# Optimization experiments

Measured on AMD Instinct MI355X. Metric: run time of the kernel, lower is better.

Reference implementation:

```python
import jax, jax.numpy as jnp
import numpy as np

B = 8192        # batch
OBS = 256       # obs_dim
ACT = 32        # action_dim -> output is 2*ACT (mu, log_std)
HID = 512       # hidden_dim
P = 8           # number of base policies (experts)
LOG_STD_MIN, LOG_STD_MAX = -5.0, 2.0


def setup_inputs() -> dict:
    key = jax.random.key(0)
    ks = jax.random.split(key, 14)
    s = 0.05
    return {
        "obs": jax.random.normal(ks[0], (B, OBS), dtype=jnp.float32),
        # gate network: obs -> HID -> HID -> P (softmax)
        "gw0": jax.random.normal(ks[1], (HID, OBS), dtype=jnp.float32) * s,
        "gb0": jnp.zeros((HID,), dtype=jnp.float32),
        "gw1": jax.random.normal(ks[2], (HID, HID), dtype=jnp.float32) * s,
        "gb1": jnp.zeros((HID,), dtype=jnp.float32),
        "gw2": jax.random.normal(ks[3], (P, HID), dtype=jnp.float32) * s,
        "gb2": jnp.zeros((P,), dtype=jnp.float32),
        # stacked expert (base-policy) trunk params, hidden_depth=2
        "ew0": jax.random.normal(ks[4], (P, HID, OBS), dtype=jnp.float32) * s,
        "eb0": jax.random.normal(ks[5], (P, HID), dtype=jnp.float32) * s,
        "ew1": jax.random.normal(ks[6], (P, HID, HID), dtype=jnp.float32) * s,
        "eb1": jax.random.normal(ks[7], (P, HID), dtype=jnp.float32) * s,
        "ew2": jax.random.normal(ks[8], (P, 2 * ACT, HID), dtype=jnp.float32) * s,
        "eb2": jax.random.normal(ks[9], (P, 2 * ACT), dtype=jnp.float32) * s,
    }


def _blend_linear(blend, W, b, x):
    # Math identical to: W_new = reshape(blend @ flatten(W,1)); bmm(W_new, x) + blend @ b
    # Contracted in the efficient order (per-expert GEMM then blend): [B,P,out] intermediate.
    y = jnp.einsum('bp,poi,bi->bo', blend, W, x, optimize=True)
    return y + blend @ b


def reference(obs, gw0, gb0, gw1, gb1, gw2, gb2, ew0, eb0, ew1, eb1, ew2, eb2):
    # gate network with softmax output
    h = jax.nn.relu(obs @ gw0.T + gb0)
    h = jax.nn.relu(h @ gw1.T + gb1)
    blend = jax.nn.softmax(h @ gw2.T + gb2, axis=-1)  # [B, P]

    # blended per-sample MLP (hidden_depth = 2)
    x = jax.nn.relu(_blend_linear(blend, ew0, eb0, obs))
    x = jax.nn.relu(_blend_linear(blend, ew1, eb1, x))
    x = _blend_linear(blend, ew2, eb2, x)  # [B, 2*ACT]

    mu, log_std = jnp.split(x, 2, axis=-1)
    log_std = jnp.tanh(log_std)
    log_std = LOG_STD_MIN + 0.5 * (LOG_STD_MAX - LOG_STD_MIN) * (log_std + 1.0)
    std = jnp.exp(log_std)
    # dist = SquashedNormal(mu, std); return its defining tensors
    return jnp.concatenate([mu, std], axis=-1)
```

## Files before the change

kernel.cpp:

```cpp
#include <hip/hip_runtime.h>
#include <hip/hip_bf16.h>
#include <cstdint>
#include <cstddef>

#define B_DIM   8192
#define OBS_DIM 256
#define ACT_DIM 32
#define HID_DIM 512
#define NEXPERT 8

typedef __attribute__((ext_vector_type(4))) float        f32x4;
typedef __attribute__((ext_vector_type(8))) short        s16x8;
typedef __attribute__((ext_vector_type(4))) unsigned int u32x4;

__device__ __forceinline__ unsigned cvt_pk_bf16(float lo, float hi) {
    unsigned r;
    asm("v_cvt_pk_bf16_f32 %0, %1, %2" : "=v"(r) : "v"(lo), "v"(hi));
    return r;
}
__device__ __forceinline__ float bf16_lo_f32(unsigned u) { return __uint_as_float(u << 16); }
__device__ __forceinline__ float bf16_hi_f32(unsigned u) { return __uint_as_float(u & 0xffff0000u); }

struct CvtArgs {
    const float*    s[7];
    unsigned short* d[7];
    int             nb[7];
};

__global__ __launch_bounds__(256) void cvt_multi(CvtArgs a) {
    int bid = blockIdx.x;
    int seg = 0, base = 0;
    while (seg < 6 && bid >= base + a.nb[seg]) { base += a.nb[seg]; ++seg; }
    int local = (bid - base) * 256 + threadIdx.x;
    const f32x4* s = (const f32x4*)a.s[seg];
    f32x4 v0 = s[local * 2 + 0];
    f32x4 v1 = s[local * 2 + 1];
    u32x4 o;
    o[0] = cvt_pk_bf16(v0[0], v0[1]);
    o[1] = cvt_pk_bf16(v0[2], v0[3]);
    o[2] = cvt_pk_bf16(v1[0], v1[1]);
    o[3] = cvt_pk_bf16(v1[2], v1[3]);
    ((u32x4*)a.d[seg])[local] = o;
}

__global__ __launch_bounds__(256) void gate_softmax(const unsigned short* __restrict__ h1,
                                                    const unsigned short* __restrict__ gw2,
                                                    const float* __restrict__ gb2,
                                                    float* __restrict__ blend) {
    const int lane = threadIdx.x & 63;
    const int wid  = threadIdx.x >> 6;
    const int row  = blockIdx.x * 4 + wid;

    u32x4 xv = *(const u32x4*)(h1 + (size_t)row * HID_DIM + lane * 8);
    float x[8];
#pragma unroll
    for (int j = 0; j < 4; ++j) {
        unsigned u   = xv[j];
        x[2 * j]     = bf16_lo_f32(u);
        x[2 * j + 1] = bf16_hi_f32(u);
    }
    float s[NEXPERT];
#pragma unroll
    for (int pp = 0; pp < NEXPERT; ++pp) {
        u32x4 wv = *(const u32x4*)(gw2 + (size_t)pp * HID_DIM + lane * 8);
        float d  = 0.f;
#pragma unroll
        for (int j = 0; j < 4; ++j) {
            unsigned u = wv[j];
            d += x[2 * j] * bf16_lo_f32(u);
            d += x[2 * j + 1] * bf16_hi_f32(u);
        }
        s[pp] = d;
    }
#pragma unroll
    for (int off = 1; off < 64; off <<= 1) {
#pragma unroll
        for (int pp = 0; pp < NEXPERT; ++pp) s[pp] += __shfl_xor(s[pp], off);
    }
    if (lane == 0) {
        float l[NEXPERT], m = -1e30f;
#pragma unroll
        for (int pp = 0; pp < NEXPERT; ++pp) { l[pp] = s[pp] + gb2[pp]; m = fmaxf(m, l[pp]); }
        float sum = 0.f;
#pragma unroll
        for (int pp = 0; pp < NEXPERT; ++pp) { l[pp] = __expf(l[pp] - m); sum += l[pp]; }
        float inv = 1.f / sum;
#pragma unroll
        for (int pp = 0; pp < NEXPERT; ++pp) blend[(size_t)row * NEXPERT + pp] = l[pp] * inv;
    }
}

template <int KIN, int NOUT>
__global__ __launch_bounds__(256, 2) void gemm_gate(const unsigned short* __restrict__ A,
                                                    const unsigned short* __restrict__ W,
                                                    const float* __restrict__ bias,
                                                    unsigned short* __restrict__ outb) {
    constexpr int BM = 128, BN = 64, BK = 64;

    __shared__ unsigned short sA[BM * BK];
    __shared__ unsigned short sB[BN * BK];

    const int t    = threadIdx.x;
    const int lane = t & 63;
    const int wid  = t >> 6;
    const int wm   = wid >> 1, wn = wid & 1;
    const int m0   = blockIdx.x * BM;
    const int n0   = blockIdx.y * BN;

    f32x4 acc[4][2];
#pragma unroll
    for (int i = 0; i < 4; ++i)
#pragma unroll
        for (int j = 0; j < 2; ++j) acc[i][j] = {0.f, 0.f, 0.f, 0.f};

#pragma unroll 1
    for (int kt = 0; kt < KIN / BK; ++kt) {
        const int ks = kt * BK;
        __syncthreads();
        const unsigned short* Wp = W + (size_t)n0 * KIN + ks;
#pragma unroll
        for (int c = 0; c < 2; ++c) {
            const int ch  = c * 256 + t;
            const int row = ch >> 3;
            const int gs  = (ch & 7) ^ (row & 7);
            __builtin_amdgcn_global_load_lds(
                (const __attribute__((address_space(1))) unsigned int*)(Wp + (size_t)row * KIN + gs * 8),
                (__attribute__((address_space(3))) unsigned int*)(sB + ch * 8), 16, 0, 0);
        }
        const unsigned short* Ap = A + (size_t)m0 * KIN + ks;
#pragma unroll
        for (int c = 0; c < 4; ++c) {
            const int ch  = c * 256 + t;
            const int row = ch >> 3;
            const int gs  = (ch & 7) ^ (row & 7);
            __builtin_amdgcn_global_load_lds(
                (const __attribute__((address_space(1))) unsigned int*)(Ap + (size_t)row * KIN + gs * 8),
                (__attribute__((address_space(3))) unsigned int*)(sA + ch * 8), 16, 0, 0);
        }
        __syncthreads();

#pragma unroll
        for (int kk = 0; kk < BK; kk += 32) {
            const int kb = kk + ((lane >> 4) << 3);
            s16x8 af[4], bfr[2];
#pragma unroll
            for (int mf = 0; mf < 4; ++mf) {
                const int row = wm * 64 + mf * 16 + (lane & 15);
                const int idx = (row * BK + kb) ^ ((row & 7) << 3);
                af[mf] = *(const s16x8*)(sA + idx);
            }
#pragma unroll
            for (int nf = 0; nf < 2; ++nf) {
                const int row = wn * 32 + nf * 16 + (lane & 15);
                const int idx = (row * BK + kb) ^ ((row & 7) << 3);
                bfr[nf] = *(const s16x8*)(sB + idx);
            }
#pragma unroll
            for (int mf = 0; mf < 4; ++mf)
#pragma unroll
                for (int nf = 0; nf < 2; ++nf)
                    acc[mf][nf] = __builtin_amdgcn_mfma_f32_16x16x32_bf16(af[mf], bfr[nf],
                                                                          acc[mf][nf], 0, 0, 0);
        }
    }

    const int cn = lane & 15;
    const int rb = (lane >> 4) << 2;
#pragma unroll
    for (int nf = 0; nf < 2; ++nf) {
        const int gn   = n0 + wn * 32 + nf * 16 + cn;
        const float bv = bias[gn];
#pragma unroll
        for (int mf = 0; mf < 4; ++mf) {
#pragma unroll
            for (int r = 0; r < 4; ++r) {
                const int gm = m0 + wm * 64 + mf * 16 + rb + r;
                float v = fmaxf(acc[mf][nf][r] + bv, 0.f);
                outb[(size_t)gm * NOUT + gn] = (unsigned short)(cvt_pk_bf16(v, v) & 0xffffu);
            }
        }
    }
}

template <int KIN, int NOUT, int BN, int KTILES>
__global__ __launch_bounds__(256, 2) void gemm_moe_sk(const unsigned short* __restrict__ A,
                                                      const unsigned short* __restrict__ W,
                                                      const float* __restrict__ blend,
                                                      float* __restrict__ part) {
    constexpr int BM   = 128, BK = 64;
    constexpr int NF   = BN / 32;
    constexpr int EXPT = KIN / BK;
    constexpr int NPE  = KTILES / EXPT;
    static_assert(KTILES % EXPT == 0, "split must align to expert boundary");

    __shared__ unsigned short sA[BM * BK];
    __shared__ unsigned short sB[BN * BK];

    const int t    = threadIdx.x;
    const int lane = t & 63;
    const int wid  = t >> 6;
    const int wm   = wid >> 1, wn = wid & 1;
    const int m0   = blockIdx.x * BM;
    const int n0   = blockIdx.y * BN;
    const int sp   = blockIdx.z;

    const int cn = lane & 15;
    const int rb = (lane >> 4) << 2;

    f32x4 mast[4][NF];
#pragma unroll
    for (int i = 0; i < 4; ++i)
#pragma unroll
        for (int j = 0; j < NF; ++j) mast[i][j] = {0.f, 0.f, 0.f, 0.f};

#pragma unroll 1
    for (int pe = 0; pe < NPE; ++pe) {
        const int p = sp * NPE + pe;
        f32x4 eacc[4][NF];
#pragma unroll
        for (int i = 0; i < 4; ++i)
#pragma unroll
            for (int j = 0; j < NF; ++j) eacc[i][j] = {0.f, 0.f, 0.f, 0.f};

        const unsigned short* Ap0 = A + (size_t)m0 * KIN;
        const unsigned short* Wp0 = W + ((size_t)p * NOUT + n0) * KIN;

#pragma unroll 1
        for (int kt = 0; kt < EXPT; ++kt) {
            const int ks = kt * BK;
            __syncthreads();
#pragma unroll
            for (int c = 0; c < NF; ++c) {
                const int ch  = c * 256 + t;
                const int row = ch >> 3;
                const int gs  = (ch & 7) ^ (row & 7);
                __builtin_amdgcn_global_load_lds(
                    (const __attribute__((address_space(1))) unsigned int*)(Wp0 + (size_t)row * KIN + ks + gs * 8),
                    (__attribute__((address_space(3))) unsigned int*)(sB + ch * 8), 16, 0, 0);
            }
#pragma unroll
            for (int c = 0; c < 4; ++c) {
                const int ch  = c * 256 + t;
                const int row = ch >> 3;
                const int gs  = (ch & 7) ^ (row & 7);
                __builtin_amdgcn_global_load_lds(
                    (const __attribute__((address_space(1))) unsigned int*)(Ap0 + (size_t)row * KIN + ks + gs * 8),
                    (__attribute__((address_space(3))) unsigned int*)(sA + ch * 8), 16, 0, 0);
            }
            __syncthreads();

#pragma unroll
            for (int kk = 0; kk < BK; kk += 32) {
                const int kb = kk + ((lane >> 4) << 3);
                s16x8 af[4], bfr[NF];
#pragma unroll
                for (int mf = 0; mf < 4; ++mf) {
                    const int row = wm * 64 + mf * 16 + (lane & 15);
                    const int idx = (row * BK + kb) ^ ((row & 7) << 3);
                    af[mf] = *(const s16x8*)(sA + idx);
                }
#pragma unroll
                for (int nf = 0; nf < NF; ++nf) {
                    const int row = wn * (BN / 2) + nf * 16 + (lane & 15);
                    const int idx = (row * BK + kb) ^ ((row & 7) << 3);
                    bfr[nf] = *(const s16x8*)(sB + idx);
                }
#pragma unroll
                for (int mf = 0; mf < 4; ++mf)
#pragma unroll
                    for (int nf = 0; nf < NF; ++nf)
                        eacc[mf][nf] = __builtin_amdgcn_mfma_f32_16x16x32_bf16(af[mf], bfr[nf],
                                                                               eacc[mf][nf], 0, 0, 0);
            }
        }

#pragma unroll
        for (int mf = 0; mf < 4; ++mf) {
#pragma unroll
            for (int r = 0; r < 4; ++r) {
                const int gm = m0 + wm * 64 + mf * 16 + rb + r;
                const float bl = blend[(size_t)gm * NEXPERT + p];
#pragma unroll
                for (int nf = 0; nf < NF; ++nf)
                    mast[mf][nf][r] += bl * eacc[mf][nf][r];
            }
        }
    }

    float* dst = part + (size_t)sp * B_DIM * NOUT;
#pragma unroll
    for (int mf = 0; mf < 4; ++mf) {
#pragma unroll
        for (int r = 0; r < 4; ++r) {
            const int gm = m0 + wm * 64 + mf * 16 + rb + r;
#pragma unroll
            for (int nf = 0; nf < NF; ++nf) {
                const int gn = n0 + wn * (BN / 2) + nf * 16 + cn;
                dst[(size_t)gm * NOUT + gn] = mast[mf][nf][r];
            }
        }
    }
}

__global__ __launch_bounds__(256) void reduce2_relu(const float* __restrict__ part,
                                                    const float* __restrict__ blend,
                                                    const float* __restrict__ eb,
                                                    unsigned short* __restrict__ out) {
    const int tid = blockIdx.x * 256 + threadIdx.x;
    const int row = tid >> 6;
    const int c0  = (tid & 63) << 3;

    const f32x4* p0 = (const f32x4*)(part + (size_t)row * HID_DIM + c0);
    const f32x4* p1 = (const f32x4*)(part + ((size_t)B_DIM + row) * HID_DIM + c0);
    f32x4 v0 = p0[0], v1 = p0[1], w0 = p1[0], w1 = p1[1];

    const f32x4* bl = (const f32x4*)(blend + (size_t)row * NEXPERT);
    const f32x4 b0 = bl[0], b1 = bl[1];
    const float blv[8] = {b0[0], b0[1], b0[2], b0[3], b1[0], b1[1], b1[2], b1[3]};

    float res[8];
#pragma unroll
    for (int j = 0; j < 4; ++j) { res[j] = v0[j] + w0[j]; res[4 + j] = v1[j] + w1[j]; }
#pragma unroll
    for (int pp = 0; pp < NEXPERT; ++pp) {
        const f32x4* e = (const f32x4*)(eb + (size_t)pp * HID_DIM + c0);
        const f32x4 e0 = e[0], e1 = e[1];
#pragma unroll
        for (int j = 0; j < 4; ++j) {
            res[j]     += blv[pp] * e0[j];
            res[4 + j] += blv[pp] * e1[j];
        }
    }
    u32x4 o;
#pragma unroll
    for (int j = 0; j < 4; ++j)
        o[j] = cvt_pk_bf16(fmaxf(res[2 * j], 0.f), fmaxf(res[2 * j + 1], 0.f));
    *(u32x4*)(out + (size_t)row * HID_DIM + c0) = o;
}

__global__ __launch_bounds__(256) void reduce8_head(const float* __restrict__ part,
                                                    const float* __restrict__ blend,
                                                    const float* __restrict__ eb2,
                                                    float* __restrict__ out) {
    const int tid = blockIdx.x * 256 + threadIdx.x;
    const int row = tid >> 3;
    const int c0  = (tid & 7) << 3;

    float res[8] = {0.f, 0.f, 0.f, 0.f, 0.f, 0.f, 0.f, 0.f};
#pragma unroll
    for (int sp = 0; sp < 8; ++sp) {
        const f32x4* ps = (const f32x4*)(part + ((size_t)sp * B_DIM + row) * 64 + c0);
        const f32x4 a = ps[0], b = ps[1];
#pragma unroll
        for (int j = 0; j < 4; ++j) { res[j] += a[j]; res[4 + j] += b[j]; }
    }
    const f32x4* bl = (const f32x4*)(blend + (size_t)row * NEXPERT);
    const f32x4 b0 = bl[0], b1 = bl[1];
    const float blv[8] = {b0[0], b0[1], b0[2], b0[3], b1[0], b1[1], b1[2], b1[3]};
#pragma unroll
    for (int pp = 0; pp < NEXPERT; ++pp) {
        const f32x4* e = (const f32x4*)(eb2 + (size_t)pp * 64 + c0);
        const f32x4 e0 = e[0], e1 = e[1];
#pragma unroll
        for (int j = 0; j < 4; ++j) {
            res[j]     += blv[pp] * e0[j];
            res[4 + j] += blv[pp] * e1[j];
        }
    }
    f32x4 o0, o1;
#pragma unroll
    for (int j = 0; j < 8; ++j) {
        const int col = c0 + j;
        float v = res[j];
        if (col >= ACT_DIM) {
            const float vc = fminf(fmaxf(v, -15.f), 15.f);
            const float e2 = __expf(2.f * vc);
            const float th = (e2 - 1.f) / (e2 + 1.f);
            v = __expf(-1.5f + 3.5f * th);
        }
        if (j < 4) o0[j] = v; else o1[j - 4] = v;
    }
    f32x4* dst = (f32x4*)(out + (size_t)row * 64 + c0);
    dst[0] = o0;
    dst[1] = o1;
}

extern "C" void kernel_launch(void* const* d_in, const int* in_sizes, int n_in,
                              void* d_out, int out_size, void* d_ws, size_t ws_size,
                              hipStream_t stream) {
    const float* obs = (const float*)d_in[0];
    const float* gw0 = (const float*)d_in[1];
    const float* gb0 = (const float*)d_in[2];
    const float* gw1 = (const float*)d_in[3];
    const float* gb1 = (const float*)d_in[4];
    const float* gw2 = (const float*)d_in[5];
    const float* gb2 = (const float*)d_in[6];
    const float* ew0 = (const float*)d_in[7];
    const float* eb0 = (const float*)d_in[8];
    const float* ew1 = (const float*)d_in[9];
    const float* eb1 = (const float*)d_in[10];
    const float* ew2 = (const float*)d_in[11];
    const float* eb2 = (const float*)d_in[12];

    char* w = (char*)d_ws;
    auto alloc = [&](size_t bytes) {
        char* r = w;
        w += (bytes + 255) & ~(size_t)255;
        return r;
    };
    unsigned short* obs_bf = (unsigned short*)alloc((size_t)B_DIM * OBS_DIM * 2);
    unsigned short* gw0_bf = (unsigned short*)alloc((size_t)HID_DIM * OBS_DIM * 2);
    unsigned short* gw1_bf = (unsigned short*)alloc((size_t)HID_DIM * HID_DIM * 2);
    unsigned short* gw2_bf = (unsigned short*)alloc((size_t)NEXPERT * HID_DIM * 2);
    unsigned short* ew0_bf = (unsigned short*)alloc((size_t)NEXPERT * HID_DIM * OBS_DIM * 2);
    unsigned short* ew1_bf = (unsigned short*)alloc((size_t)NEXPERT * HID_DIM * HID_DIM * 2);
    unsigned short* ew2_bf = (unsigned short*)alloc((size_t)NEXPERT * 2 * ACT_DIM * HID_DIM * 2);
    unsigned short* h0     = (unsigned short*)alloc((size_t)B_DIM * HID_DIM * 2);
    unsigned short* h1     = (unsigned short*)alloc((size_t)B_DIM * HID_DIM * 2);
    float*          blend  = (float*)alloc((size_t)B_DIM * NEXPERT * 4);
    float*          part   = (float*)alloc((size_t)2 * B_DIM * HID_DIM * 4);

    CvtArgs ca;
    ca.s[0] = obs; ca.d[0] = obs_bf; ca.nb[0] = (B_DIM * OBS_DIM / 8) / 256;
    ca.s[1] = gw0; ca.d[1] = gw0_bf; ca.nb[1] = (HID_DIM * OBS_DIM / 8) / 256;
    ca.s[2] = gw1; ca.d[2] = gw1_bf; ca.nb[2] = (HID_DIM * HID_DIM / 8) / 256;
    ca.s[3] = gw2; ca.d[3] = gw2_bf; ca.nb[3] = (NEXPERT * HID_DIM / 8) / 256;
    ca.s[4] = ew0; ca.d[4] = ew0_bf; ca.nb[4] = (NEXPERT * HID_DIM * OBS_DIM / 8) / 256;
    ca.s[5] = ew1; ca.d[5] = ew1_bf; ca.nb[5] = (NEXPERT * HID_DIM * HID_DIM / 8) / 256;
    ca.s[6] = ew2; ca.d[6] = ew2_bf; ca.nb[6] = (NEXPERT * 64 * HID_DIM / 8) / 256;
    int total_blocks = 0;
    for (int i = 0; i < 7; ++i) total_blocks += ca.nb[i];
    cvt_multi<<<total_blocks, 256, 0, stream>>>(ca);

    gemm_gate<OBS_DIM, HID_DIM><<<dim3(B_DIM / 128, HID_DIM / 64), 256, 0, stream>>>(
        obs_bf, gw0_bf, gb0, h0);
    gemm_gate<HID_DIM, HID_DIM><<<dim3(B_DIM / 128, HID_DIM / 64), 256, 0, stream>>>(
        h0, gw1_bf, gb1, h1);
    gate_softmax<<<B_DIM / 4, 256, 0, stream>>>(h1, gw2_bf, gb2, blend);

    gemm_moe_sk<OBS_DIM, HID_DIM, 128, 16><<<dim3(B_DIM / 128, HID_DIM / 128, 2), 256, 0, stream>>>(
        obs_bf, ew0_bf, blend, part);
    reduce2_relu<<<B_DIM * 64 / 256, 256, 0, stream>>>(part, blend, eb0, h0);

    gemm_moe_sk<HID_DIM, HID_DIM, 128, 32><<<dim3(B_DIM / 128, HID_DIM / 128, 2), 256, 0, stream>>>(
        h0, ew1_bf, blend, part);
    reduce2_relu<<<B_DIM * 64 / 256, 256, 0, stream>>>(part, blend, eb1, h1);

    gemm_moe_sk<HID_DIM, 64, 64, 8><<<dim3(B_DIM / 128, 1, 8), 256, 0, stream>>>(
        h1, ew2_bf, blend, part);
    reduce8_head<<<B_DIM * 8 / 256, 256, 0, stream>>>(part, blend, eb2, (float*)d_out);
}
```

Before: 214.8 us.

## Fuse all stages into one persistent kernel with software grid barriers

Replaces the ten separate launches (convert, two gate GEMMs, softmax, three MoE GEMMs, three reductions) with a single persistent kernel of 512 blocks. The stages are separated by atomic-counter grid barriers, and each block strides over its virtual blocks. The aim is to remove per-launch overhead and the gaps between dependent kernels. The risks are barrier spin cost and a dependence on all 512 blocks being co-resident at two blocks per CU. The barrier also has a timeout break that could silently race if co-residency fails.

```diff
diff --git a/kernel.cpp b/kernel.cpp
--- a/kernel.cpp
+++ b/kernel.cpp
@@ -8,6 +8,7 @@
 #define ACT_DIM 32
 #define HID_DIM 512
 #define NEXPERT 8
+#define GRID    512
 
 typedef __attribute__((ext_vector_type(4))) float        f32x4;
 typedef __attribute__((ext_vector_type(8))) short        s16x8;
@@ -21,91 +22,68 @@
 __device__ __forceinline__ float bf16_lo_f32(unsigned u) { return __uint_as_float(u << 16); }
 __device__ __forceinline__ float bf16_hi_f32(unsigned u) { return __uint_as_float(u & 0xffff0000u); }
 
-struct CvtArgs {
-    const float*    s[7];
-    unsigned short* d[7];
-    int             nb[7];
+struct MegaArgs {
+    const float*    cs[7];
+    unsigned short* cd[7];
+    int             cnb[7];
+    int             ctot;
+    const unsigned short *obs_bf, *gw0_bf, *gw1_bf, *gw2_bf, *ew0_bf, *ew1_bf, *ew2_bf;
+    const float *gb0, *gb1, *gb2, *eb0, *eb1, *eb2;
+    unsigned short *h0, *h1;
+    float *blend, *part, *out;
+    unsigned *bar;
 };
 
-__global__ __launch_bounds__(256) void cvt_multi(CvtArgs a) {
-    int bid = blockIdx.x;
-    int seg = 0, base = 0;
-    while (seg < 6 && bid >= base + a.nb[seg]) { base += a.nb[seg]; ++seg; }
-    int local = (bid - base) * 256 + threadIdx.x;
-    const f32x4* s = (const f32x4*)a.s[seg];
-    f32x4 v0 = s[local * 2 + 0];
-    f32x4 v1 = s[local * 2 + 1];
-    u32x4 o;
-    o[0] = cvt_pk_bf16(v0[0], v0[1]);
-    o[1] = cvt_pk_bf16(v0[2], v0[3]);
-    o[2] = cvt_pk_bf16(v1[0], v1[1]);
-    o[3] = cvt_pk_bf16(v1[2], v1[3]);
-    ((u32x4*)a.d[seg])[local] = o;
-}
-
-__global__ __launch_bounds__(256) void gate_softmax(const unsigned short* __restrict__ h1,
-                                                    const unsigned short* __restrict__ gw2,
-                                                    const float* __restrict__ gb2,
-                                                    float* __restrict__ blend) {
-    const int lane = threadIdx.x & 63;
-    const int wid  = threadIdx.x >> 6;
-    const int row  = blockIdx.x * 4 + wid;
-
-    u32x4 xv = *(const u32x4*)(h1 + (size_t)row * HID_DIM + lane * 8);
-    float x[8];
-#pragma unroll
-    for (int j = 0; j < 4; ++j) {
-        unsigned u   = xv[j];
-        x[2 * j]     = bf16_lo_f32(u);
-        x[2 * j + 1] = bf16_hi_f32(u);
-    }
-    float s[NEXPERT];
-#pragma unroll
-    for (int pp = 0; pp < NEXPERT; ++pp) {
-        u32x4 wv = *(const u32x4*)(gw2 + (size_t)pp * HID_DIM + lane * 8);
-        float d  = 0.f;
-#pragma unroll
-        for (int j = 0; j < 4; ++j) {
-            unsigned u = wv[j];
-            d += x[2 * j] * bf16_lo_f32(u);
-            d += x[2 * j + 1] * bf16_hi_f32(u);
-        }
-        s[pp] = d;
-    }
-#pragma unroll
-    for (int off = 1; off < 64; off <<= 1) {
-#pragma unroll
-        for (int pp = 0; pp < NEXPERT; ++pp) s[pp] += __shfl_xor(s[pp], off);
-    }
-    if (lane == 0) {
-        float l[NEXPERT], m = -1e30f;
-#pragma unroll
-        for (int pp = 0; pp < NEXPERT; ++pp) { l[pp] = s[pp] + gb2[pp]; m = fmaxf(m, l[pp]); }
-        float sum = 0.f;
-#pragma unroll
-        for (int pp = 0; pp < NEXPERT; ++pp) { l[pp] = __expf(l[pp] - m); sum += l[pp]; }
-        float inv = 1.f / sum;
-#pragma unroll
-        for (int pp = 0; pp < NEXPERT; ++pp) blend[(size_t)row * NEXPERT + pp] = l[pp] * inv;
+__device__ __forceinline__ void grid_barrier(unsigned* ctr) {
+    __syncthreads();
+    if (threadIdx.x == 0) {
+        __threadfence();
+        atomicAdd(ctr, 1u);
+        const long long t0 = clock64();
+        while (__hip_atomic_load(ctr, __ATOMIC_RELAXED, __HIP_MEMORY_SCOPE_AGENT)
+               < (unsigned)GRID) {
+            __builtin_amdgcn_s_sleep(2);
+            if (clock64() - t0 > (1LL << 26)) break;
+        }
+        __threadfence();
+    }
+    __syncthreads();
+}
+
+__device__ void cvt_stage(int b, const MegaArgs& a) {
+    const int t = threadIdx.x;
+    for (int vb = b; vb < a.ctot; vb += GRID) {
+        int seg = 0, base = 0;
+        while (seg < 6 && vb >= base + a.cnb[seg]) { base += a.cnb[seg]; ++seg; }
+        const int local = (vb - base) * 256 + t;
+        const f32x4* s = (const f32x4*)a.cs[seg];
+        f32x4 v0 = s[local * 2 + 0];
+        f32x4 v1 = s[local * 2 + 1];
+        u32x4 o;
+        o[0] = cvt_pk_bf16(v0[0], v0[1]);
+        o[1] = cvt_pk_bf16(v0[2], v0[3]);
+        o[2] = cvt_pk_bf16(v1[0], v1[1]);
+        o[3] = cvt_pk_bf16(v1[2], v1[3]);
+        ((u32x4*)a.cd[seg])[local] = o;
     }
 }
 
 template <int KIN, int NOUT>
-__global__ __launch_bounds__(256, 2) void gemm_gate(const unsigned short* __restrict__ A,
-                                                    const unsigned short* __restrict__ W,
-                                                    const float* __restrict__ bias,
-                                                    unsigned short* __restrict__ outb) {
+__device__ void gate_stage(int b, const unsigned short* __restrict__ A,
+                           const unsigned short* __restrict__ W,
+                           const float* __restrict__ bias,
+                           unsigned short* __restrict__ outb,
+                           unsigned char* SMEM) {
     constexpr int BM = 128, BN = 64, BK = 64;
-
-    __shared__ unsigned short sA[BM * BK];
-    __shared__ unsigned short sB[BN * BK];
+    unsigned short* sA = (unsigned short*)SMEM;
+    unsigned short* sB = (unsigned short*)(SMEM + BM * BK * 2);
 
     const int t    = threadIdx.x;
     const int lane = t & 63;
     const int wid  = t >> 6;
     const int wm   = wid >> 1, wn = wid & 1;
-    const int m0   = blockIdx.x * BM;
-    const int n0   = blockIdx.y * BN;
+    const int m0   = (b & 63) * BM;
+    const int n0   = (b >> 6) * BN;
 
     f32x4 acc[4][2];
 #pragma unroll
@@ -182,27 +160,77 @@
     }
 }
 
-template <int KIN, int NOUT, int BN, int KTILES>
-__global__ __launch_bounds__(256, 2) void gemm_moe_sk(const unsigned short* __restrict__ A,
-                                                      const unsigned short* __restrict__ W,
-                                                      const float* __restrict__ blend,
-                                                      float* __restrict__ part) {
-    constexpr int BM   = 128, BK = 64;
-    constexpr int NF   = BN / 32;
-    constexpr int EXPT = KIN / BK;
-    constexpr int NPE  = KTILES / EXPT;
-    static_assert(KTILES % EXPT == 0, "split must align to expert boundary");
-
-    __shared__ unsigned short sA[BM * BK];
-    __shared__ unsigned short sB[BN * BK];
+__device__ void softmax_stage(int b, const unsigned short* __restrict__ h1,
+                              const unsigned short* __restrict__ gw2,
+                              const float* __restrict__ gb2,
+                              float* __restrict__ blend) {
+    const int lane = threadIdx.x & 63;
+    const int wid  = threadIdx.x >> 6;
+    for (int vb = b; vb < B_DIM / 4; vb += GRID) {
+        const int row = vb * 4 + wid;
+        u32x4 xv = *(const u32x4*)(h1 + (size_t)row * HID_DIM + lane * 8);
+        float x[8];
+#pragma unroll
+        for (int j = 0; j < 4; ++j) {
+            unsigned u   = xv[j];
+            x[2 * j]     = bf16_lo_f32(u);
+            x[2 * j + 1] = bf16_hi_f32(u);
+        }
+        float s[NEXPERT];
+#pragma unroll
+        for (int pp = 0; pp < NEXPERT; ++pp) {
+            u32x4 wv = *(const u32x4*)(gw2 + (size_t)pp * HID_DIM + lane * 8);
+            float d  = 0.f;
+#pragma unroll
+            for (int j = 0; j < 4; ++j) {
+                unsigned u = wv[j];
+                d += x[2 * j] * bf16_lo_f32(u);
+                d += x[2 * j + 1] * bf16_hi_f32(u);
+            }
+            s[pp] = d;
+        }
+#pragma unroll
+        for (int off = 1; off < 64; off <<= 1) {
+#pragma unroll
+            for (int pp = 0; pp < NEXPERT; ++pp) s[pp] += __shfl_xor(s[pp], off);
+        }
+        if (lane == 0) {
+            float l[NEXPERT], m = -1e30f;
+#pragma unroll
+            for (int pp = 0; pp < NEXPERT; ++pp) { l[pp] = s[pp] + gb2[pp]; m = fmaxf(m, l[pp]); }
+            float sum = 0.f;
+#pragma unroll
+            for (int pp = 0; pp < NEXPERT; ++pp) { l[pp] = __expf(l[pp] - m); sum += l[pp]; }
+            float inv = 1.f / sum;
+#pragma unroll
+            for (int pp = 0; pp < NEXPERT; ++pp) blend[(size_t)row * NEXPERT + pp] = l[pp] * inv;
+        }
+    }
+}
+
+template <int KIN, int NOUT, int BN, int TPB>
+__device__ void moe_stage(int b, const unsigned short* __restrict__ A,
+                          const unsigned short* __restrict__ W,
+                          const float* __restrict__ blend,
+                          float* __restrict__ part,
+                          unsigned char* SMEM) {
+    constexpr int BM  = 128, BK = 64;
+    constexpr int NF  = BN / 32;
+    constexpr int TPE = KIN / BK;
+    constexpr int NPE = (TPB >= TPE) ? TPB / TPE : 1;
+    constexpr int ET  = (TPB >= TPE) ? TPE : TPB;
+    static_assert((TPB % TPE == 0) || (TPE % TPB == 0), "split/expert alignment");
+
+    unsigned short* sA = (unsigned short*)SMEM;
+    unsigned short* sB = (unsigned short*)(SMEM + BM * BK * 2);
 
     const int t    = threadIdx.x;
     const int lane = t & 63;
     const int wid  = t >> 6;
     const int wm   = wid >> 1, wn = wid & 1;
-    const int m0   = blockIdx.x * BM;
-    const int n0   = blockIdx.y * BN;
-    const int sp   = blockIdx.z;
+    const int m0 = (b & 63) * BM;
+    const int n0 = (NOUT == 64) ? 0 : ((b >> 6) & 3) * BN;
+    const int sp = (NOUT == 64) ? (b >> 6) : (b >> 8);
 
     const int cn = lane & 15;
     const int rb = (lane >> 4) << 2;
@@ -215,18 +243,21 @@
 
 #pragma unroll 1
     for (int pe = 0; pe < NPE; ++pe) {
-        const int p = sp * NPE + pe;
+        const int tbase = sp * TPB + pe * ET;
+        const int p     = tbase / TPE;
+        const int ksb   = (tbase % TPE) * BK;
+
         f32x4 eacc[4][NF];
 #pragma unroll
         for (int i = 0; i < 4; ++i)
 #pragma unroll
             for (int j = 0; j < NF; ++j) eacc[i][j] = {0.f, 0.f, 0.f, 0.f};
 
-        const unsigned short* Ap0 = A + (size_t)m0 * KIN;
-        const unsigned short* Wp0 = W + ((size_t)p * NOUT + n0) * KIN;
+        const unsigned short* Ap0 = A + (size_t)m0 * KIN + ksb;
+        const unsigned short* Wp0 = W + ((size_t)p * NOUT + n0) * KIN + ksb;
 
 #pragma unroll 1
-        for (int kt = 0; kt < EXPT; ++kt) {
+        for (int kt = 0; kt < ET; ++kt) {
             const int ks = kt * BK;
             __syncthreads();
 #pragma unroll
@@ -302,87 +333,116 @@
     }
 }
 
-__global__ __launch_bounds__(256) void reduce2_relu(const float* __restrict__ part,
-                                                    const float* __restrict__ blend,
-                                                    const float* __restrict__ eb,
-                                                    unsigned short* __restrict__ out) {
-    const int tid = blockIdx.x * 256 + threadIdx.x;
-    const int row = tid >> 6;
-    const int c0  = (tid & 63) << 3;
-
-    const f32x4* p0 = (const f32x4*)(part + (size_t)row * HID_DIM + c0);
-    const f32x4* p1 = (const f32x4*)(part + ((size_t)B_DIM + row) * HID_DIM + c0);
-    f32x4 v0 = p0[0], v1 = p0[1], w0 = p1[0], w1 = p1[1];
-
-    const f32x4* bl = (const f32x4*)(blend + (size_t)row * NEXPERT);
-    const f32x4 b0 = bl[0], b1 = bl[1];
-    const float blv[8] = {b0[0], b0[1], b0[2], b0[3], b1[0], b1[1], b1[2], b1[3]};
-
-    float res[8];
-#pragma unroll
-    for (int j = 0; j < 4; ++j) { res[j] = v0[j] + w0[j]; res[4 + j] = v1[j] + w1[j]; }
-#pragma unroll
-    for (int pp = 0; pp < NEXPERT; ++pp) {
-        const f32x4* e = (const f32x4*)(eb + (size_t)pp * HID_DIM + c0);
-        const f32x4 e0 = e[0], e1 = e[1];
-#pragma unroll
-        for (int j = 0; j < 4; ++j) {
-            res[j]     += blv[pp] * e0[j];
-            res[4 + j] += blv[pp] * e1[j];
-        }
-    }
-    u32x4 o;
-#pragma unroll
-    for (int j = 0; j < 4; ++j)
-        o[j] = cvt_pk_bf16(fmaxf(res[2 * j], 0.f), fmaxf(res[2 * j + 1], 0.f));
-    *(u32x4*)(out + (size_t)row * HID_DIM + c0) = o;
-}
-
-__global__ __launch_bounds__(256) void reduce8_head(const float* __restrict__ part,
-                                                    const float* __restrict__ blend,
-                                                    const float* __restrict__ eb2,
-                                                    float* __restrict__ out) {
-    const int tid = blockIdx.x * 256 + threadIdx.x;
-    const int row = tid >> 3;
-    const int c0  = (tid & 7) << 3;
-
-    float res[8] = {0.f, 0.f, 0.f, 0.f, 0.f, 0.f, 0.f, 0.f};
-#pragma unroll
-    for (int sp = 0; sp < 8; ++sp) {
-        const f32x4* ps = (const f32x4*)(part + ((size_t)sp * B_DIM + row) * 64 + c0);
-        const f32x4 a = ps[0], b = ps[1];
-#pragma unroll
-        for (int j = 0; j < 4; ++j) { res[j] += a[j]; res[4 + j] += b[j]; }
-    }
-    const f32x4* bl = (const f32x4*)(blend + (size_t)row * NEXPERT);
-    const f32x4 b0 = bl[0], b1 = bl[1];
-    const float blv[8] = {b0[0], b0[1], b0[2], b0[3], b1[0], b1[1], b1[2], b1[3]};
-#pragma unroll
-    for (int pp = 0; pp < NEXPERT; ++pp) {
-        const f32x4* e = (const f32x4*)(eb2 + (size_t)pp * 64 + c0);
-        const f32x4 e0 = e[0], e1 = e[1];
-#pragma unroll
-        for (int j = 0; j < 4; ++j) {
-            res[j]     += blv[pp] * e0[j];
-            res[4 + j] += blv[pp] * e1[j];
-        }
-    }
-    f32x4 o0, o1;
-#pragma unroll
-    for (int j = 0; j < 8; ++j) {
-        const int col = c0 + j;
-        float v = res[j];
-        if (col >= ACT_DIM) {
-            const float vc = fminf(fmaxf(v, -15.f), 15.f);
-            const float e2 = __expf(2.f * vc);
-            const float th = (e2 - 1.f) / (e2 + 1.f);
-            v = __expf(-1.5f + 3.5f * th);
-        }
-        if (j < 4) o0[j] = v; else o1[j - 4] = v;
-    }
-    f32x4* dst = (f32x4*)(out + (size_t)row * 64 + c0);
-    dst[0] = o0;
-    dst[1] = o1;
+__device__ void reduce2_stage(int b, const float* __restrict__ part,
+                              const float* __restrict__ blend,
+                              const float* __restrict__ eb,
+                              unsigned short* __restrict__ out) {
+    for (int vb = b; vb < B_DIM * 64 / 256; vb += GRID) {
+        const int tid = vb * 256 + threadIdx.x;
+        const int row = tid >> 6;
+        const int c0  = (tid & 63) << 3;
+
+        const f32x4* p0 = (const f32x4*)(part + (size_t)row * HID_DIM + c0);
+        const f32x4* p1 = (const f32x4*)(part + ((size_t)B_DIM + row) * HID_DIM + c0);
+        f32x4 v0 = p0[0], v1 = p0[1], w0 = p1[0], w1 = p1[1];
+
+        const f32x4* bl = (const f32x4*)(blend + (size_t)row * NEXPERT);
+        const f32x4 b0 = bl[0], b1 = bl[1];
+        const float blv[8] = {b0[0], b0[1], b0[2], b0[3], b1[0], b1[1], b1[2], b1[3]};
+
+        float res[8];
+#pragma unroll
+        for (int j = 0; j < 4; ++j) { res[j] = v0[j] + w0[j]; res[4 + j] = v1[j] + w1[j]; }
+#pragma unroll
+        for (int pp = 0; pp < NEXPERT; ++pp) {
+            const f32x4* e = (const f32x4*)(eb + (size_t)pp * HID_DIM + c0);
+            const f32x4 e0 = e[0], e1 = e[1];
+#pragma unroll
+            for (int j = 0; j < 4; ++j) {
+                res[j]     += blv[pp] * e0[j];
+                res[4 + j] += blv[pp] * e1[j];
+            }
+        }
+        u32x4 o;
+#pragma unroll
+        for (int j = 0; j < 4; ++j)
+            o[j] = cvt_pk_bf16(fmaxf(res[2 * j], 0.f), fmaxf(res[2 * j + 1], 0.f));
+        *(u32x4*)(out + (size_t)row * HID_DIM + c0) = o;
+    }
+}
+
+__device__ void reduce8_stage(int b, const float* __restrict__ part,
+                              const float* __restrict__ blend,
+                              const float* __restrict__ eb2,
+                              float* __restrict__ out) {
+    for (int vb = b; vb < B_DIM * 8 / 256; vb += GRID) {
+        const int tid = vb * 256 + threadIdx.x;
+        const int row = tid >> 3;
+        const int c0  = (tid & 7) << 3;
+
+        float res[8] = {0.f, 0.f, 0.f, 0.f, 0.f, 0.f, 0.f, 0.f};
+#pragma unroll
+        for (int sp = 0; sp < 8; ++sp) {
+            const f32x4* ps = (const f32x4*)(part + ((size_t)sp * B_DIM + row) * 64 + c0);
+            const f32x4 a = ps[0], bb = ps[1];
+#pragma unroll
+            for (int j = 0; j < 4; ++j) { res[j] += a[j]; res[4 + j] += bb[j]; }
+        }
+        const f32x4* bl = (const f32x4*)(blend + (size_t)row * NEXPERT);
+        const f32x4 b0 = bl[0], b1 = bl[1];
+        const float blv[8] = {b0[0], b0[1], b0[2], b0[3], b1[0], b1[1], b1[2], b1[3]};
+#pragma unroll
+        for (int pp = 0; pp < NEXPERT; ++pp) {
+            const f32x4* e = (const f32x4*)(eb2 + (size_t)pp * 64 + c0);
+            const f32x4 e0 = e[0], e1 = e[1];
+#pragma unroll
+            for (int j = 0; j < 4; ++j) {
+                res[j]     += blv[pp] * e0[j];
+                res[4 + j] += blv[pp] * e1[j];
+            }
+        }
+        f32x4 o0, o1;
+#pragma unroll
+        for (int j = 0; j < 8; ++j) {
+            const int col = c0 + j;
+            float v = res[j];
+            if (col >= ACT_DIM) {
+                const float vc = fminf(fmaxf(v, -15.f), 15.f);
+                const float e2 = __expf(2.f * vc);
+                const float th = (e2 - 1.f) / (e2 + 1.f);
+                v = __expf(-1.5f + 3.5f * th);
+            }
+            if (j < 4) o0[j] = v; else o1[j - 4] = v;
+        }
+        f32x4* dst = (f32x4*)(out + (size_t)row * 64 + c0);
+        dst[0] = o0;
+        dst[1] = o1;
+    }
+}
+
+__global__ __launch_bounds__(256, 2) void mega(MegaArgs a) {
+    __shared__ __align__(16) unsigned char SMEM[32768];
+    const int b = blockIdx.x;
+
+    cvt_stage(b, a);
+    grid_barrier(&a.bar[0]);
+    gate_stage<OBS_DIM, HID_DIM>(b, a.obs_bf, a.gw0_bf, a.gb0, a.h0, SMEM);
+    grid_barrier(&a.bar[1]);
+    gate_stage<HID_DIM, HID_DIM>(b, a.h0, a.gw1_bf, a.gb1, a.h1, SMEM);
+    grid_barrier(&a.bar[2]);
+    softmax_stage(b, a.h1, a.gw2_bf, a.gb2, a.blend);
+    grid_barrier(&a.bar[3]);
+    moe_stage<OBS_DIM, HID_DIM, 128, 16>(b, a.obs_bf, a.ew0_bf, a.blend, a.part, SMEM);
+    grid_barrier(&a.bar[4]);
+    reduce2_stage(b, a.part, a.blend, a.eb0, a.h0);
+    grid_barrier(&a.bar[5]);
+    moe_stage<HID_DIM, HID_DIM, 128, 32>(b, a.h0, a.ew1_bf, a.blend, a.part, SMEM);
+    grid_barrier(&a.bar[6]);
+    reduce2_stage(b, a.part, a.blend, a.eb1, a.h1);
+    grid_barrier(&a.bar[7]);
+    moe_stage<HID_DIM, 64, 64, 8>(b, a.h1, a.ew2_bf, a.blend, a.part, SMEM);
+    grid_barrier(&a.bar[8]);
+    reduce8_stage(b, a.part, a.blend, a.eb2, a.out);
 }
 
 extern "C" void kernel_launch(void* const* d_in, const int* in_sizes, int n_in,
@@ -408,6 +468,7 @@
         w += (bytes + 255) & ~(size_t)255;
         return r;
     };
+    unsigned*       bar    = (unsigned*)alloc(16 * sizeof(unsigned));
     unsigned short* obs_bf = (unsigned short*)alloc((size_t)B_DIM * OBS_DIM * 2);
     unsigned short* gw0_bf = (unsigned short*)alloc((size_t)HID_DIM * OBS_DIM * 2);
     unsigned short* gw1_bf = (unsigned short*)alloc((size_t)HID_DIM * HID_DIM * 2);
@@ -420,33 +481,25 @@
     float*          blend  = (float*)alloc((size_t)B_DIM * NEXPERT * 4);
     float*          part   = (float*)alloc((size_t)2 * B_DIM * HID_DIM * 4);
 
-    CvtArgs ca;
-    ca.s[0] = obs; ca.d[0] = obs_bf; ca.nb[0] = (B_DIM * OBS_DIM / 8) / 256;
-    ca.s[1] = gw0; ca.d[1] = gw0_bf; ca.nb[1] = (HID_DIM * OBS_DIM / 8) / 256;
-    ca.s[2] = gw1; ca.d[2] = gw1_bf; ca.nb[2] = (HID_DIM * HID_DIM / 8) / 256;
-    ca.s[3] = gw2; ca.d[3] = gw2_bf; ca.nb[3] = (NEXPERT * HID_DIM / 8) / 256;
-    ca.s[4] = ew0; ca.d[4] = ew0_bf; ca.nb[4] = (NEXPERT * HID_DIM * OBS_DIM / 8) / 256;
-    ca.s[5] = ew1; ca.d[5] = ew1_bf; ca.nb[5] = (NEXPERT * HID_DIM * HID_DIM / 8) / 256;
-    ca.s[6] = ew2; ca.d[6] = ew2_bf; ca.nb[6] = (NEXPERT * 64 * HID_DIM / 8) / 256;
-    int total_blocks = 0;
-    for (int i = 0; i < 7; ++i) total_blocks += ca.nb[i];
-    cvt_multi<<<total_blocks, 256, 0, stream>>>(ca);
-
-    gemm_gate<OBS_DIM, HID_DIM><<<dim3(B_DIM / 128, HID_DIM / 64), 256, 0, stream>>>(
-        obs_bf, gw0_bf, gb0, h0);
-    gemm_gate<HID_DIM, HID_DIM><<<dim3(B_DIM / 128, HID_DIM / 64), 256, 0, stream>>>(
-        h0, gw1_bf, gb1, h1);
-    gate_softmax<<<B_DIM / 4, 256, 0, stream>>>(h1, gw2_bf, gb2, blend);
-
-    gemm_moe_sk<OBS_DIM, HID_DIM, 128, 16><<<dim3(B_DIM / 128, HID_DIM / 128, 2), 256, 0, stream>>>(
-        obs_bf, ew0_bf, blend, part);
-    reduce2_relu<<<B_DIM * 64 / 256, 256, 0, stream>>>(part, blend, eb0, h0);
-
-    gemm_moe_sk<HID_DIM, HID_DIM, 128, 32><<<dim3(B_DIM / 128, HID_DIM / 128, 2), 256, 0, stream>>>(
-        h0, ew1_bf, blend, part);
-    reduce2_relu<<<B_DIM * 64 / 256, 256, 0, stream>>>(part, blend, eb1, h1);
-
-    gemm_moe_sk<HID_DIM, 64, 64, 8><<<dim3(B_DIM / 128, 1, 8), 256, 0, stream>>>(
-        h1, ew2_bf, blend, part);
-    reduce8_head<<<B_DIM * 8 / 256, 256, 0, stream>>>(part, blend, eb2, (float*)d_out);
-}
+    hipMemsetAsync(bar, 0, 16 * sizeof(unsigned), stream);
+
+    MegaArgs ma;
+    ma.cs[0] = obs; ma.cd[0] = obs_bf; ma.cnb[0] = (B_DIM * OBS_DIM / 8) / 256;
+    ma.cs[1] = gw0; ma.cd[1] = gw0_bf; ma.cnb[1] = (HID_DIM * OBS_DIM / 8) / 256;
+    ma.cs[2] = gw1; ma.cd[2] = gw1_bf; ma.cnb[2] = (HID_DIM * HID_DIM / 8) / 256;
+    ma.cs[3] = gw2; ma.cd[3] = gw2_bf; ma.cnb[3] = (NEXPERT * HID_DIM / 8) / 256;
+    ma.cs[4] = ew0; ma.cd[4] = ew0_bf; ma.cnb[4] = (NEXPERT * HID_DIM * OBS_DIM / 8) / 256;
+    ma.cs[5] = ew1; ma.cd[5] = ew1_bf; ma.cnb[5] = (NEXPERT * HID_DIM * HID_DIM / 8) / 256;
+    ma.cs[6] = ew2; ma.cd[6] = ew2_bf; ma.cnb[6] = (NEXPERT * 64 * HID_DIM / 8) / 256;
+    ma.ctot = 0;
+    for (int i = 0; i < 7; ++i) ma.ctot += ma.cnb[i];
+    ma.obs_bf = obs_bf; ma.gw0_bf = gw0_bf; ma.gw1_bf = gw1_bf; ma.gw2_bf = gw2_bf;
+    ma.ew0_bf = ew0_bf; ma.ew1_bf = ew1_bf; ma.ew2_bf = ew2_bf;
+    ma.gb0 = gb0; ma.gb1 = gb1; ma.gb2 = gb2;
+    ma.eb0 = eb0; ma.eb1 = eb1; ma.eb2 = eb2;
+    ma.h0 = h0; ma.h1 = h1;
+    ma.blend = blend; ma.part = part; ma.out = (float*)d_out;
+    ma.bar = bar;
+
+    mega<<<dim3(GRID), dim3(256), 0, stream>>>(ma);
+}
```

Result: slower. 742.1 us (+245.5%).
